# Kernel tuning notes

Hardware: AMD Instinct MI355X
Metric: run time of the kernel (lower is better)

The kernel has to match this reference:

```python
import jax, jax.numpy as jnp
import numpy as np

E, N, HID, NH = 250000, 50000, 128, 4
HD = HID // NH  # head_dim = 32


def setup_inputs() -> dict:
    key = jax.random.key(0)
    ks = jax.random.split(key, 16)
    f = lambda k, s: jax.random.normal(k, s, dtype=jnp.float32)
    w = lambda k, s: jax.random.normal(k, s, dtype=jnp.float32) * 0.05
    return {
        "edge_attr": f(ks[0], (E, HID)),
        "node_features": f(ks[1], (N, HID)),
        "regime_probs": jax.random.uniform(ks[2], (3,), dtype=jnp.float32),
        # phase_query / phase_key: Linear(hidden+3 -> hidden)
        "Wq": w(ks[3], (HID, HID + 3)), "bq": jnp.zeros((HID,), jnp.float32),
        "Wk": w(ks[4], (HID, HID + 3)), "bk": jnp.zeros((HID,), jnp.float32),
        # phase_value: Linear(hidden -> hidden)
        "Wv": w(ks[5], (HID, HID)), "bv": jnp.zeros((HID,), jnp.float32),
        # nn.MultiheadAttention packed in-projection [3*hid, hid] and out_proj
        "W_in": w(ks[6], (3 * HID, HID)), "b_in": jnp.zeros((3 * HID,), jnp.float32),
        "W_mo": w(ks[7], (HID, HID)), "b_mo": jnp.zeros((HID,), jnp.float32),
        # output_proj
        "Wo": w(ks[8], (HID, HID)), "bo": jnp.zeros((HID,), jnp.float32),
        "edge_index": jax.random.randint(ks[9], (2, E), 0, N, dtype=jnp.int64),
    }


def reference(edge_attr, node_features, regime_probs,
              Wq, bq, Wk, bk, Wv, bv,
              W_in, b_in, W_mo, b_mo, Wo, bo,
              edge_index):
    e = edge_attr.shape[0]
    src = node_features[edge_index[0]]  # [E, HID] gather
    tgt = node_features[edge_index[1]]  # [E, HID] gather
    reg = jnp.broadcast_to(regime_probs, (e, regime_probs.shape[0]))  # [E, 3]

    q = jnp.concatenate([src, reg], axis=1) @ Wq.T + bq  # [E, HID]
    k = jnp.concatenate([tgt, reg], axis=1) @ Wk.T + bk  # [E, HID]
    v = edge_attr @ Wv.T + bv                             # [E, HID]

    # nn.MultiheadAttention with seq_len 1 (batch_first): in-proj, heads, softmax, out-proj
    Wiq, Wik, Wiv = jnp.split(W_in, 3, axis=0)
    biq, bik, biv = jnp.split(b_in, 3)
    q2 = (q @ Wiq.T + biq).reshape(e, NH, HD)
    k2 = (k @ Wik.T + bik).reshape(e, NH, HD)
    v2 = (v @ Wiv.T + biv).reshape(e, NH, HD)

    scale = 1.0 / jnp.sqrt(jnp.float32(HD))
    scores = jnp.sum(q2 * k2, axis=-1, keepdims=True) * scale  # [E, NH, 1]
    probs = jax.nn.softmax(scores, axis=-1)                    # seq-len-1 -> all ones
    att = (probs * v2).reshape(e, HID)                         # == v2 merged
    att = att @ W_mo.T + b_mo                                  # MHA out_proj

    out = att @ Wo.T + bo                                      # output_proj
    return edge_attr + 0.5 * out
```

## Files before the change

kernel.cpp:

```cpp
#include <hip/hip_runtime.h>
#include <hip/hip_bf16.h>

#define HID 128

typedef __attribute__((ext_vector_type(8))) short short8;
typedef __attribute__((ext_vector_type(4))) float f32x4;

static __device__ __forceinline__ short f2bf(float x) {
    __hip_bfloat16 h = __float2bfloat16(x);
    return *reinterpret_cast<short*>(&h);
}

__global__ void prep_products(const float* __restrict__ Wo,
                              const float* __restrict__ W_mo,
                              const float* __restrict__ Wiv,
                              const float* __restrict__ Wv,
                              const float* __restrict__ bv,
                              const float* __restrict__ biv,
                              const float* __restrict__ b_mo,
                              const float* __restrict__ bo,
                              float* __restrict__ Pl,
                              float* __restrict__ Pr,
                              float* __restrict__ cv)
{
    const int j = threadIdx.x;
    const int b = blockIdx.x;
    __shared__ float sh[HID];

    if (b < 256) {
        const float* A = (b < 128) ? Wo   : Wiv;
        const float* B = (b < 128) ? W_mo : Wv;
        float*       C = (b < 128) ? Pl   : Pr;
        const int i = b & 127;
        sh[j] = A[i * HID + j];
        __syncthreads();
        float s = 0.f;
        #pragma unroll 16
        for (int k = 0; k < HID; ++k) s += sh[k] * B[k * HID + j];
        C[i * HID + j] = s;
    } else {
        sh[j] = bv[j];
        __syncthreads();
        float t = biv[j];
        #pragma unroll 16
        for (int k = 0; k < HID; ++k) t += Wiv[j * HID + k] * sh[k];
        __syncthreads(); sh[j] = t; __syncthreads();
        t = b_mo[j];
        #pragma unroll 16
        for (int k = 0; k < HID; ++k) t += W_mo[j * HID + k] * sh[k];
        __syncthreads(); sh[j] = t; __syncthreads();
        t = bo[j];
        #pragma unroll 16
        for (int k = 0; k < HID; ++k) t += Wo[j * HID + k] * sh[k];
        cv[j] = 0.5f * t;
    }
}

__global__ void prep_final(const float* __restrict__ Pl,
                           const float* __restrict__ Pr,
                           __hip_bfloat16* __restrict__ Mb)
{
    const int i = blockIdx.x, j = threadIdx.x;
    __shared__ float sh[HID];
    sh[j] = Pl[i * HID + j];
    __syncthreads();
    float s = 0.f;
    #pragma unroll 16
    for (int k = 0; k < HID; ++k) s += sh[k] * Pr[k * HID + j];
    Mb[i * HID + j] = __float2bfloat16(((i == j) ? 1.0f : 0.0f) + 0.5f * s);
}

__global__ __launch_bounds__(256) void edge_gemm(
    const float* __restrict__ ea,
    const __hip_bfloat16* __restrict__ Mb,
    const float* __restrict__ cvec,
    float* __restrict__ out,
    int E, int numTiles)
{
    const int lane  = threadIdx.x & 63;
    const int wv    = threadIdx.x >> 6;
    const int q     = lane >> 4;
    const int c     = lane & 15;
    const int ncol0 = wv * 32;

    short8 Mfrag[2][4];
    #pragma unroll
    for (int nt = 0; nt < 2; ++nt) {
        const __hip_bfloat16* mp = Mb + (size_t)(ncol0 + nt * 16 + c) * HID + q * 8;
        #pragma unroll
        for (int kk = 0; kk < 4; ++kk)
            Mfrag[nt][kk] = *reinterpret_cast<const short8*>(mp + kk * 32);
    }
    f32x4 cvp[2];
    #pragma unroll
    for (int nt = 0; nt < 2; ++nt)
        cvp[nt] = *reinterpret_cast<const f32x4*>(cvec + ncol0 + nt * 16 + q * 4);

    int t = blockIdx.x;
    if (t >= numTiles) return;

    float4 raw[8];
    {
        int row = t * 16 + c; if (row > E - 1) row = E - 1;
        const float* ap = ea + (size_t)row * HID + q * 8;
        #pragma unroll
        for (int kk = 0; kk < 4; ++kk) {
            raw[2 * kk]     = *reinterpret_cast<const float4*>(ap + kk * 32);
            raw[2 * kk + 1] = *reinterpret_cast<const float4*>(ap + kk * 32 + 4);
        }
    }

    while (true) {
        const int edge0 = t * 16;
        const int tn    = t + gridDim.x;

        short8 bfrag[4];
        #pragma unroll
        for (int kk = 0; kk < 4; ++kk) {
            const float4 f0 = raw[2 * kk], f1 = raw[2 * kk + 1];
            short8 v;
            v[0] = f2bf(f0.x); v[1] = f2bf(f0.y); v[2] = f2bf(f0.z); v[3] = f2bf(f0.w);
            v[4] = f2bf(f1.x); v[5] = f2bf(f1.y); v[6] = f2bf(f1.z); v[7] = f2bf(f1.w);
            bfrag[kk] = v;
        }

        if (tn < numTiles) {
            int row = tn * 16 + c; if (row > E - 1) row = E - 1;
            const float* ap = ea + (size_t)row * HID + q * 8;
            #pragma unroll
            for (int kk = 0; kk < 4; ++kk) {
                raw[2 * kk]     = *reinterpret_cast<const float4*>(ap + kk * 32);
                raw[2 * kk + 1] = *reinterpret_cast<const float4*>(ap + kk * 32 + 4);
            }
        }

        f32x4 acc[2] = { cvp[0], cvp[1] };
        #pragma unroll
        for (int kk = 0; kk < 4; ++kk) {
            acc[0] = __builtin_amdgcn_mfma_f32_16x16x32_bf16(Mfrag[0][kk], bfrag[kk], acc[0], 0, 0, 0);
            acc[1] = __builtin_amdgcn_mfma_f32_16x16x32_bf16(Mfrag[1][kk], bfrag[kk], acc[1], 0, 0, 0);
        }

        const int orow = edge0 + c;
        if (orow < E) {
            float* op = out + (size_t)orow * HID + ncol0 + q * 4;
            __builtin_nontemporal_store(acc[0], reinterpret_cast<f32x4*>(op));
            __builtin_nontemporal_store(acc[1], reinterpret_cast<f32x4*>(op + 16));
        }

        if (tn >= numTiles) break;
        t = tn;
    }
}

extern "C" void kernel_launch(void* const* d_in, const int* in_sizes, int n_in,
                              void* d_out, int out_size, void* d_ws, size_t ws_size,
                              hipStream_t stream) {
    const float* Wv   = (const float*)d_in[7];
    const float* bv   = (const float*)d_in[8];
    const float* W_in = (const float*)d_in[9];
    const float* b_in = (const float*)d_in[10];
    const float* W_mo = (const float*)d_in[11];
    const float* b_mo = (const float*)d_in[12];
    const float* Wo   = (const float*)d_in[13];
    const float* bo   = (const float*)d_in[14];
    const float* Wiv  = W_in + 2 * HID * HID;
    const float* biv  = b_in + 2 * HID;

    char* ws = (char*)d_ws;
    float*          Pl = (float*)(ws);
    float*          Pr = (float*)(ws + 65536);
    __hip_bfloat16* Mb = (__hip_bfloat16*)(ws + 131072);
    float*          cv = (float*)(ws + 163840);

    const int E = in_sizes[0] / HID;
    const int numTiles = (E + 15) / 16;
    const int grid = numTiles < 2048 ? numTiles : 2048;

    prep_products<<<dim3(257), dim3(HID), 0, stream>>>(
        Wo, W_mo, Wiv, Wv, bv, biv, b_mo, bo, Pl, Pr, cv);
    prep_final<<<dim3(HID), dim3(HID), 0, stream>>>(Pl, Pr, Mb);

    edge_gemm<<<dim3(grid), dim3(256), 0, stream>>>(
        (const float*)d_in[0], Mb, cv, (float*)d_out, E, numTiles);
}
```

Before: 298.0 us.

## Stage edge_attr tiles cooperatively into swizzled double-buffered LDS via global_load_lds

Previously each of the four waves in a block loaded the full 16-row edge_attr tile into registers, so every row was fetched four times through the vector memory path. The kernel now has each wave fetch a quarter of the tile straight into LDS with global_load_lds, using an XOR swizzle and two buffers so the next tile's load overlaps the current tile's compute. Waves then read their bf16 fragments from LDS. This cuts redundant global and L2 traffic at the cost of 16 KB of LDS per block, a per-tile barrier, and a vmcnt wait that relies on the stores being the only later outstanding vector-memory operations.

```diff
diff --git a/kernel.cpp b/kernel.cpp
--- a/kernel.cpp
+++ b/kernel.cpp
@@ -77,6 +77,8 @@
     float* __restrict__ out,
     int E, int numTiles)
 {
+    __shared__ __align__(16) float lds[2][2048];
+
     const int lane  = threadIdx.x & 63;
     const int wv    = threadIdx.x >> 6;
     const int q     = lane >> 4;
@@ -99,39 +101,49 @@
     int t = blockIdx.x;
     if (t >= numTiles) return;
 
-    float4 raw[8];
-    {
-        int row = t * 16 + c; if (row > E - 1) row = E - 1;
-        const float* ap = ea + (size_t)row * HID + q * 8;
-        #pragma unroll
-        for (int kk = 0; kk < 4; ++kk) {
-            raw[2 * kk]     = *reinterpret_cast<const float4*>(ap + kk * 32);
-            raw[2 * kk + 1] = *reinterpret_cast<const float4*>(ap + kk * 32 + 4);
-        }
-    }
-
+    const int swz   = (c & 7) << 4;
+    const int rbase = c * 512 + ((q * 32) ^ (swz & 0x60));
+    const int hx    = swz & 16;
+
+    auto stage_tile = [&](float* ldsbuf, int edge0) {
+        #pragma unroll
+        for (int j = 0; j < 2; ++j) {
+            const int i = wv * 2 + j;
+            const int r = i * 2 + (lane >> 5);
+            const int b = ((lane & 31) * 16) ^ ((r & 7) << 4);
+            int grow = edge0 + r; if (grow > E - 1) grow = E - 1;
+            const char* src = (const char*)ea + (size_t)grow * 512 + b;
+            float* dst = ldsbuf + i * 256;
+            __builtin_amdgcn_global_load_lds(
+                (const __attribute__((address_space(1))) void*)src,
+                (__attribute__((address_space(3))) void*)dst,
+                16, 0, 0);
+        }
+    };
+
+    stage_tile(&lds[0][0], t * 16);
+    asm volatile("s_waitcnt vmcnt(0)" ::: "memory");
+    __builtin_amdgcn_s_barrier();
+    __builtin_amdgcn_sched_barrier(0);
+
+    int cur = 0;
     while (true) {
         const int edge0 = t * 16;
         const int tn    = t + gridDim.x;
-
+        const bool has_next = (tn < numTiles);
+
+        if (has_next) stage_tile(&lds[cur ^ 1][0], tn * 16);
+
+        const char* lb = (const char*)&lds[cur][0];
         short8 bfrag[4];
         #pragma unroll
         for (int kk = 0; kk < 4; ++kk) {
-            const float4 f0 = raw[2 * kk], f1 = raw[2 * kk + 1];
+            const float4 f0 = *reinterpret_cast<const float4*>(lb + rbase + kk * 128 + hx);
+            const float4 f1 = *reinterpret_cast<const float4*>(lb + rbase + kk * 128 + (16 ^ hx));
             short8 v;
             v[0] = f2bf(f0.x); v[1] = f2bf(f0.y); v[2] = f2bf(f0.z); v[3] = f2bf(f0.w);
             v[4] = f2bf(f1.x); v[5] = f2bf(f1.y); v[6] = f2bf(f1.z); v[7] = f2bf(f1.w);
             bfrag[kk] = v;
-        }
-
-        if (tn < numTiles) {
-            int row = tn * 16 + c; if (row > E - 1) row = E - 1;
-            const float* ap = ea + (size_t)row * HID + q * 8;
-            #pragma unroll
-            for (int kk = 0; kk < 4; ++kk) {
-                raw[2 * kk]     = *reinterpret_cast<const float4*>(ap + kk * 32);
-                raw[2 * kk + 1] = *reinterpret_cast<const float4*>(ap + kk * 32 + 4);
-            }
         }
 
         f32x4 acc[2] = { cvp[0], cvp[1] };
@@ -148,7 +160,13 @@
             __builtin_nontemporal_store(acc[1], reinterpret_cast<f32x4*>(op + 16));
         }
 
-        if (tn >= numTiles) break;
+        if (!has_next) break;
+
+        asm volatile("s_waitcnt vmcnt(2)" ::: "memory");
+        __builtin_amdgcn_s_barrier();
+        __builtin_amdgcn_sched_barrier(0);
+
+        cur ^= 1;
         t = tn;
     }
 }
```

New measurement: 283.7 us. 4.8% less time.
